# Kernel optimization log

Measured on AMD Instinct MI355X. Metric: run time of the kernel, lower is better.

## Reference

```python
import jax, jax.numpy as jnp
import numpy as np

IN_DIM, OUT_DIM = 256, 64
N_WNODES, N_PNODES, N_EDGES = 100000, 50000, 1600000


def setup_inputs() -> dict:
    key = jax.random.key(0)
    k_h, k_src, k_dst, k_fc, k_attn = jax.random.split(key, 5)
    h = jax.random.normal(k_h, (N_WNODES, IN_DIM), dtype=jnp.float32)
    edge_src = jax.random.randint(k_src, (N_EDGES,), 0, N_WNODES)
    edge_dst = jax.random.randint(k_dst, (N_EDGES,), 0, N_PNODES)
    W_fc = jax.random.normal(k_fc, (IN_DIM, OUT_DIM), dtype=jnp.float32) / np.sqrt(IN_DIM)
    # attn_fc: Linear(2*out_dim, 1, bias=False) -> weight vector of length 2*OUT_DIM
    W_attn = jax.random.normal(k_attn, (2 * OUT_DIM,), dtype=jnp.float32) / np.sqrt(2 * OUT_DIM)
    return {"h": h, "edge_src": edge_src, "edge_dst": edge_dst,
            "n_pnodes": N_PNODES, "W_fc": W_fc, "W_attn": W_attn}


def reference(h, edge_src, edge_dst, n_pnodes, W_fc, W_attn):
    D = W_fc.shape[1]
    z = h @ W_fc                                  # [Nw, D]
    z_src = z[edge_src]                           # [E, D] gather (memory-bound)
    # In the original, only word nodes get 'z'; DGL zero-fills dst 'z', so the
    # dst half of attn_fc contributes nothing: e = leaky_relu(z_src @ a_src + 0 @ a_dst)
    a_src = W_attn[:D]
    e = jax.nn.leaky_relu(z_src @ a_src)          # [E], slope 0.01 matches torch default
    # reduce_func masks zero-valued scores (DGL mailbox padding) with -1000
    e = jnp.where(e == 0.0, -1000.0, e)
    # segment softmax over incoming edges of each destination node
    e_max = jax.ops.segment_max(e, edge_dst, num_segments=n_pnodes)
    e_max = jnp.where(jnp.isfinite(e_max), e_max, 0.0)  # guard empty segments
    w = jnp.exp(e - e_max[edge_dst])              # [E]
    denom = jax.ops.segment_sum(w, edge_dst, num_segments=n_pnodes)
    alpha = w / jnp.maximum(denom[edge_dst], 1e-20)
    # weighted gather-scatter aggregation: sh[dst] = sum alpha * z_src
    h_out = jax.ops.segment_sum(alpha[:, None] * z_src, edge_dst, num_segments=n_pnodes)
    return h_out                                  # [n_pnodes, D] == h[pnode_id]
```

## Files before the change

kernel.cpp:

```cpp
#include <hip/hip_runtime.h>
#include <hip/hip_bf16.h>
#include <math.h>

#define IN_DIM 256
#define OUT_DIM 64
#define CHUNK_LOG2 12
#define BK_LOG2 7
#define MAXNB 512
#define BCAP 6144

typedef __attribute__((ext_vector_type(8))) short short8v;
typedef __attribute__((ext_vector_type(4))) float f32x4;

__device__ __forceinline__ unsigned short f2bf(float f) {
    unsigned u = __float_as_uint(f);
    unsigned r = (u + 0x7fffu + ((u >> 16) & 1u)) >> 16;
    return (unsigned short)r;
}

__device__ __forceinline__ float bf2f(unsigned short b) {
    return __uint_as_float(((unsigned)b) << 16);
}

__device__ __forceinline__ float edge_score(float x) {
    float e = x > 0.0f ? x : 0.01f * x;
    if (e == 0.0f) e = -1000.0f;
    return e;
}

__global__ __launch_bounds__(256) void prep_kernel(
    const float* __restrict__ Wfc, short8v* __restrict__ wtf)
{
    const int v = blockIdx.x * 256 + threadIdx.x;
    const int ks = v >> 8;
    const int t = (v >> 6) & 3;
    const int lane = v & 63;
    const int lg = lane >> 4, lr = lane & 15;
    short8v b;
    #pragma unroll
    for (int j = 0; j < 8; ++j) {
        const int k = ks * 32 + lg * 8 + j;
        b[j] = (short)f2bf(Wfc[k * OUT_DIM + t * 16 + lr]);
    }
    wtf[v] = b;
}

__global__ __launch_bounds__(256, 3) void gemm_s_kernel(
    const float* __restrict__ h, const short8v* __restrict__ wtf,
    const float* __restrict__ Wattn, const int* __restrict__ esrc,
    const int* __restrict__ edst, unsigned short* __restrict__ z,
    float* __restrict__ s, int* __restrict__ bres, int* __restrict__ brec,
    int n_rows, int n_edges, int nb)
{
    __shared__ short hl2[64 * 256];
    const int tid = threadIdx.x;
    const int lane = tid & 63;
    const int wv = tid >> 6;
    const int lg = lane >> 4;
    const int lr = lane & 15;
    const int row0 = blockIdx.x * 64;

    const int nchunks = (n_edges + (1 << CHUNK_LOG2) - 1) >> CHUNK_LOG2;
    const bool hasChunk = blockIdx.x < nchunks;
    const bool fullChunk = hasChunk &&
        ((blockIdx.x << CHUNK_LOG2) + (1 << CHUNK_LOG2) <= n_edges);
    int4 ed[4], es[4];
    if (fullChunk) {
        const int4* ep = (const int4*)edst + (blockIdx.x << (CHUNK_LOG2 - 2));
        const int4* sp = (const int4*)esrc + (blockIdx.x << (CHUNK_LOG2 - 2));
        #pragma unroll
        for (int j = 0; j < 4; ++j) { ed[j] = ep[j * 256 + tid]; es[j] = sp[j * 256 + tid]; }
    }

    float a_attn[4];
    #pragma unroll
    for (int t = 0; t < 4; ++t) a_attn[t] = Wattn[t * 16 + lr];

    #pragma unroll
    for (int i = 0; i < 8; ++i) {
        const int q = i * 256 + tid;
        const int r = q >> 5;
        const int sl = q & 31;
        const int grow = min(row0 + r, n_rows - 1);
        const float4* hp = (const float4*)(h + (size_t)grow * IN_DIM + sl * 8);
        const float4 xa = hp[0];
        const float4 xb = hp[1];
        union { short8v v; __hip_bfloat162 h2[4]; } u;
        u.h2[0] = __float22bfloat162_rn(float2{xa.x, xa.y});
        u.h2[1] = __float22bfloat162_rn(float2{xa.z, xa.w});
        u.h2[2] = __float22bfloat162_rn(float2{xb.x, xb.y});
        u.h2[3] = __float22bfloat162_rn(float2{xb.z, xb.w});
        *(short8v*)((char*)hl2 + r * 512 + ((sl ^ (r & 31)) << 4)) = u.v;
    }
    __syncthreads();

    const int rA = wv * 16 + lr;
    const char* rbase = (const char*)hl2 + rA * 512;
    const int rsw = rA & 31;

    float svj[4] = {0.f, 0.f, 0.f, 0.f};

    #pragma unroll
    for (int hf = 0; hf < 2; ++hf) {
        short8v Bf[8][2];
        #pragma unroll
        for (int ks = 0; ks < 8; ++ks)
            #pragma unroll
            for (int tt = 0; tt < 2; ++tt)
                Bf[ks][tt] = wtf[(ks * 4 + hf * 2 + tt) * 64 + lane];

        f32x4 acc[2];
        acc[0] = (f32x4){0.f, 0.f, 0.f, 0.f};
        acc[1] = (f32x4){0.f, 0.f, 0.f, 0.f};

        #pragma unroll
        for (int ks = 0; ks < 8; ++ks) {
            const short8v av =
                *(const short8v*)(rbase + (((ks * 4 + lg) ^ rsw) << 4));
            acc[0] = __builtin_amdgcn_mfma_f32_16x16x32_bf16(av, Bf[ks][0], acc[0], 0, 0, 0);
            acc[1] = __builtin_amdgcn_mfma_f32_16x16x32_bf16(av, Bf[ks][1], acc[1], 0, 0, 0);
        }

        #pragma unroll
        for (int j = 0; j < 4; ++j) {
            const int row = row0 + wv * 16 + lg * 4 + j;
            const bool ok = row < n_rows;
            #pragma unroll
            for (int tt = 0; tt < 2; ++tt) {
                const int t = hf * 2 + tt;
                const float v = acc[tt][j];
                if (ok) z[(size_t)row * OUT_DIM + t * 16 + lr] =
                    __bfloat16_as_ushort(__float2bfloat16(v));
                svj[j] = fmaf(v, a_attn[t], svj[j]);
            }
        }
    }

    #pragma unroll
    for (int j = 0; j < 4; ++j) {
        const int row = row0 + wv * 16 + lg * 4 + j;
        float p = svj[j];
        #pragma unroll
        for (int o = 1; o < 16; o <<= 1) p += __shfl_xor(p, o);
        if (row < n_rows && lr == 0) s[row] = p;
    }

    __syncthreads();
    int* lcnt = (int*)hl2;
    int* lwoff = lcnt + MAXNB;
    if (hasChunk) {
        for (int j2 = tid; j2 < nb; j2 += 256) lcnt[j2] = 0;
        __syncthreads();
        if (fullChunk) {
            #pragma unroll
            for (int j2 = 0; j2 < 4; ++j2) {
                atomicAdd(&lcnt[ed[j2].x >> BK_LOG2], 1);
                atomicAdd(&lcnt[ed[j2].y >> BK_LOG2], 1);
                atomicAdd(&lcnt[ed[j2].z >> BK_LOG2], 1);
                atomicAdd(&lcnt[ed[j2].w >> BK_LOG2], 1);
            }
        } else {
            const int i0 = blockIdx.x << CHUNK_LOG2;
            const int i1 = min(i0 + (1 << CHUNK_LOG2), n_edges);
            for (int i = i0 + tid; i < i1; i += 256)
                atomicAdd(&lcnt[edst[i] >> BK_LOG2], 1);
        }
        __syncthreads();
        for (int j2 = tid; j2 < nb; j2 += 256) {
            const int cv = lcnt[j2];
            lwoff[j2] = cv ? (j2 * BCAP + atomicAdd(bres + j2, cv)) : 0;
        }
        __syncthreads();
        if (fullChunk) {
            #pragma unroll
            for (int j2 = 0; j2 < 4; ++j2) {
                #define EMIT(dd, ss) { \
                    const int pos = atomicAdd(&lwoff[(dd) >> BK_LOG2], 1); \
                    brec[pos] = (ss) | (((dd) & ((1 << BK_LOG2) - 1)) << 17); }
                EMIT(ed[j2].x, es[j2].x)
                EMIT(ed[j2].y, es[j2].y)
                EMIT(ed[j2].z, es[j2].z)
                EMIT(ed[j2].w, es[j2].w)
                #undef EMIT
            }
        } else {
            const int i0 = blockIdx.x << CHUNK_LOG2;
            const int i1 = min(i0 + (1 << CHUNK_LOG2), n_edges);
            for (int i = i0 + tid; i < i1; i += 256) {
                const int d = edst[i];
                const int pos = atomicAdd(&lwoff[d >> BK_LOG2], 1);
                brec[pos] = esrc[i] | ((d & ((1 << BK_LOG2) - 1)) << 17);
            }
        }
    }
}

__global__ __launch_bounds__(256) void p2_kernel(
    const int* __restrict__ bres, int* __restrict__ brec,
    int2* __restrict__ oln, int n_pnodes)
{
    __shared__ int srec[BCAP];
    __shared__ int lh[128], lsc[128], lwf[128];
    const int b = blockIdx.x;
    const int tid = threadIdx.x;
    const int base = b * BCAP;
    const int len = min(bres[b], BCAP);

    if (tid < 128) lh[tid] = 0;
    __syncthreads();
    for (int i = tid; i < len; i += 256) {
        const int r = brec[base + i];
        srec[i] = r;
        atomicAdd(&lh[r >> 17], 1);
    }
    __syncthreads();
    if (tid < 128) lsc[tid] = lh[tid];
    __syncthreads();
    for (int d = 1; d < 128; d <<= 1) {
        int v = 0;
        if (tid < 128 && tid >= d) v = lsc[tid - d];
        __syncthreads();
        if (tid < 128) lsc[tid] += v;
        __syncthreads();
    }
    const int d0 = b << BK_LOG2;
    if (tid < 128) {
        const int st = lsc[tid] - lh[tid];
        lwf[tid] = st;
        if (d0 + tid < n_pnodes)
            oln[d0 + tid] = make_int2(base + st, lh[tid]);
    }
    __syncthreads();
    for (int i = tid; i < len; i += 256) {
        const int r = srec[i];
        const int pos = atomicAdd(&lwf[r >> 17], 1);
        brec[base + pos] = r & 0x1FFFF;
    }
}

__global__ __launch_bounds__(256) void segment_kernel(
    const int2* __restrict__ oln, const int* __restrict__ ssrc,
    const float* __restrict__ s, const unsigned short* __restrict__ z,
    float* __restrict__ out, int n_pnodes)
{
    const int p = blockIdx.x * 4 + (threadIdx.x >> 6);
    if (p >= n_pnodes) return;
    const int lane = threadIdx.x & 63;
    const int2 ol = oln[p];
    const int beg = ol.x;
    const int len = ol.y;
    const int end = beg + len;

    if (len == 0) {
        out[(size_t)p * OUT_DIM + lane] = 0.0f;
        return;
    }

    float acc = 0.0f, dsum = 0.0f;

    #define GATH1(tt, wsrc, ssrcv) { \
        float wt = __shfl(wsrc, tt); \
        int st = __shfl(ssrcv, tt); \
        acc = fmaf(wt, bf2f(z[(size_t)st * OUT_DIM + lane]), acc); }
    #define GATH8(tt, wsrc, ssrcv) { \
        float w0 = __shfl(wsrc, tt),     w1 = __shfl(wsrc, tt + 1); \
        float w2 = __shfl(wsrc, tt + 2), w3 = __shfl(wsrc, tt + 3); \
        float w4 = __shfl(wsrc, tt + 4), w5 = __shfl(wsrc, tt + 5); \
        float w6 = __shfl(wsrc, tt + 6), w7 = __shfl(wsrc, tt + 7); \
        int a0 = __shfl(ssrcv, tt),     a1 = __shfl(ssrcv, tt + 1); \
        int a2 = __shfl(ssrcv, tt + 2), a3 = __shfl(ssrcv, tt + 3); \
        int a4 = __shfl(ssrcv, tt + 4), a5 = __shfl(ssrcv, tt + 5); \
        int a6 = __shfl(ssrcv, tt + 6), a7 = __shfl(ssrcv, tt + 7); \
        float z0 = bf2f(z[(size_t)a0 * OUT_DIM + lane]); \
        float z1 = bf2f(z[(size_t)a1 * OUT_DIM + lane]); \
        float z2 = bf2f(z[(size_t)a2 * OUT_DIM + lane]); \
        float z3 = bf2f(z[(size_t)a3 * OUT_DIM + lane]); \
        float z4 = bf2f(z[(size_t)a4 * OUT_DIM + lane]); \
        float z5 = bf2f(z[(size_t)a5 * OUT_DIM + lane]); \
        float z6 = bf2f(z[(size_t)a6 * OUT_DIM + lane]); \
        float z7 = bf2f(z[(size_t)a7 * OUT_DIM + lane]); \
        acc = fmaf(w0, z0, acc); acc = fmaf(w1, z1, acc); \
        acc = fmaf(w2, z2, acc); acc = fmaf(w3, z3, acc); \
        acc = fmaf(w4, z4, acc); acc = fmaf(w5, z5, acc); \
        acc = fmaf(w6, z6, acc); acc = fmaf(w7, z7, acc); }

    if (len <= 64) {
        const bool v = lane < len;
        const int j = beg + (v ? lane : 0);
        const int sr = ssrc[j];
        const float e = v ? edge_score(s[sr]) : -INFINITY;
        float m = e;
        #pragma unroll
        for (int o = 32; o > 0; o >>= 1) m = fmaxf(m, __shfl_xor(m, o));
        float w = v ? __expf(e - m) : 0.0f;
        dsum = w;
        #pragma unroll
        for (int o = 32; o > 0; o >>= 1) dsum += __shfl_xor(dsum, o);

        int t = 0;
        for (; t + 8 <= len; t += 8) GATH8(t, w, sr)
        for (; t < len; ++t) GATH1(t, w, sr)
    } else {
        float m = -INFINITY;
        for (int j = beg + lane; j < end; j += 64)
            m = fmaxf(m, edge_score(s[ssrc[j]]));
        #pragma unroll
        for (int o = 32; o > 0; o >>= 1) m = fmaxf(m, __shfl_xor(m, o));

        for (int c = beg; c < end; c += 64) {
            const int j = c + lane;
            float w = 0.0f;
            int sr = 0;
            if (j < end) {
                sr = ssrc[j];
                w = __expf(edge_score(s[sr]) - m);
            }
            dsum += w;
            const int cn = min(64, end - c);
            int t = 0;
            for (; t + 8 <= cn; t += 8) GATH8(t, w, sr)
            for (; t < cn; ++t) GATH1(t, w, sr)
        }
        #pragma unroll
        for (int o = 32; o > 0; o >>= 1) dsum += __shfl_xor(dsum, o);
    }
    #undef GATH8
    #undef GATH1

    out[(size_t)p * OUT_DIM + lane] = acc / fmaxf(dsum, 1e-20f);
}

extern "C" void kernel_launch(void* const* d_in, const int* in_sizes, int n_in,
                              void* d_out, int out_size, void* d_ws, size_t ws_size,
                              hipStream_t stream)
{
    const float* h     = (const float*)d_in[0];
    const int*   esrc  = (const int*)d_in[1];
    const int*   edst  = (const int*)d_in[2];
    const float* Wfc   = (const float*)d_in[4];
    const float* Wattn = (const float*)d_in[5];
    float* out = (float*)d_out;

    const int n_w = in_sizes[0] / IN_DIM;
    const int n_e = in_sizes[1];
    const int n_p = out_size / OUT_DIM;
    const int nb  = (n_p + (1 << BK_LOG2) - 1) >> BK_LOG2;

    short8v* wtf            = (short8v*)d_ws;
    unsigned short* z       = (unsigned short*)(wtf + 2048);
    float* s                = (float*)(z + (size_t)n_w * OUT_DIM);
    int* brec               = (int*)(s + n_w);
    int2* oln               = (int2*)(brec + (size_t)nb * BCAP);
    int* bres               = (int*)(oln + n_p);

    hipMemsetAsync(bres, 0, (size_t)nb * sizeof(int), stream);

    prep_kernel<<<8, 256, 0, stream>>>(Wfc, wtf);
    const int gemm_blocks = (n_w + 63) / 64;
    gemm_s_kernel<<<gemm_blocks, 256, 0, stream>>>(h, wtf, Wattn, esrc, edst,
                                                   z, s, bres, brec, n_w, n_e, nb);
    p2_kernel<<<nb, 256, 0, stream>>>(bres, brec, oln, n_p);
    segment_kernel<<<(n_p + 3) / 4, 256, 0, stream>>>(oln, brec, s, z, out, n_p);
}
```

Before: 111.0 us.

## Process four row tiles per GEMM block with double-buffered LDS pipelining

Result: no change. 111.1 us (+0.1%).

```diff
diff --git a/kernel.cpp b/kernel.cpp
--- a/kernel.cpp
+++ b/kernel.cpp
@@ -45,109 +45,129 @@
     wtf[v] = b;
 }
 
-__global__ __launch_bounds__(256, 3) void gemm_s_kernel(
+__global__ __launch_bounds__(256, 2) void gemm_s_kernel(
     const float* __restrict__ h, const short8v* __restrict__ wtf,
     const float* __restrict__ Wattn, const int* __restrict__ esrc,
     const int* __restrict__ edst, unsigned short* __restrict__ z,
     float* __restrict__ s, int* __restrict__ bres, int* __restrict__ brec,
     int n_rows, int n_edges, int nb)
 {
-    __shared__ short hl2[64 * 256];
+    __shared__ short hlA[64 * 256];
+    __shared__ short hlB[64 * 256];
+    __shared__ int ltab[2 * MAXNB];
     const int tid = threadIdx.x;
     const int lane = tid & 63;
     const int wv = tid >> 6;
     const int lg = lane >> 4;
     const int lr = lane & 15;
-    const int row0 = blockIdx.x * 64;
-
-    const int nchunks = (n_edges + (1 << CHUNK_LOG2) - 1) >> CHUNK_LOG2;
-    const bool hasChunk = blockIdx.x < nchunks;
-    const bool fullChunk = hasChunk &&
-        ((blockIdx.x << CHUNK_LOG2) + (1 << CHUNK_LOG2) <= n_edges);
-    int4 ed[4], es[4];
-    if (fullChunk) {
-        const int4* ep = (const int4*)edst + (blockIdx.x << (CHUNK_LOG2 - 2));
-        const int4* sp = (const int4*)esrc + (blockIdx.x << (CHUNK_LOG2 - 2));
-        #pragma unroll
-        for (int j = 0; j < 4; ++j) { ed[j] = ep[j * 256 + tid]; es[j] = sp[j * 256 + tid]; }
-    }
+    const int brow0 = blockIdx.x * 256;
+
+    short8v Bf[8][4];
+    #pragma unroll
+    for (int ks = 0; ks < 8; ++ks)
+        #pragma unroll
+        for (int t = 0; t < 4; ++t)
+            Bf[ks][t] = wtf[(ks * 4 + t) * 64 + lane];
 
     float a_attn[4];
     #pragma unroll
     for (int t = 0; t < 4; ++t) a_attn[t] = Wattn[t * 16 + lr];
 
-    #pragma unroll
-    for (int i = 0; i < 8; ++i) {
-        const int q = i * 256 + tid;
-        const int r = q >> 5;
-        const int sl = q & 31;
-        const int grow = min(row0 + r, n_rows - 1);
-        const float4* hp = (const float4*)(h + (size_t)grow * IN_DIM + sl * 8);
-        const float4 xa = hp[0];
-        const float4 xb = hp[1];
-        union { short8v v; __hip_bfloat162 h2[4]; } u;
-        u.h2[0] = __float22bfloat162_rn(float2{xa.x, xa.y});
-        u.h2[1] = __float22bfloat162_rn(float2{xa.z, xa.w});
-        u.h2[2] = __float22bfloat162_rn(float2{xb.x, xb.y});
-        u.h2[3] = __float22bfloat162_rn(float2{xb.z, xb.w});
-        *(short8v*)((char*)hl2 + r * 512 + ((sl ^ (r & 31)) << 4)) = u.v;
-    }
-    __syncthreads();
-
-    const int rA = wv * 16 + lr;
-    const char* rbase = (const char*)hl2 + rA * 512;
-    const int rsw = rA & 31;
-
-    float svj[4] = {0.f, 0.f, 0.f, 0.f};
-
-    #pragma unroll
-    for (int hf = 0; hf < 2; ++hf) {
-        short8v Bf[8][2];
-        #pragma unroll
-        for (int ks = 0; ks < 8; ++ks)
-            #pragma unroll
-            for (int tt = 0; tt < 2; ++tt)
-                Bf[ks][tt] = wtf[(ks * 4 + hf * 2 + tt) * 64 + lane];
-
-        f32x4 acc[2];
-        acc[0] = (f32x4){0.f, 0.f, 0.f, 0.f};
-        acc[1] = (f32x4){0.f, 0.f, 0.f, 0.f};
-
+    short8v sreg[8];
+
+    auto LOADT = [&](int t) {
+        #pragma unroll
+        for (int i = 0; i < 8; ++i) {
+            const int q = i * 256 + tid;
+            const int r = q >> 5;
+            const int sl = q & 31;
+            const int grow = min(brow0 + t * 64 + r, n_rows - 1);
+            const float4* hp = (const float4*)(h + (size_t)grow * IN_DIM + sl * 8);
+            const float4 xa = hp[0];
+            const float4 xb = hp[1];
+            union { short8v v; __hip_bfloat162 h2[4]; } u;
+            u.h2[0] = __float22bfloat162_rn(float2{xa.x, xa.y});
+            u.h2[1] = __float22bfloat162_rn(float2{xa.z, xa.w});
+            u.h2[2] = __float22bfloat162_rn(float2{xb.x, xb.y});
+            u.h2[3] = __float22bfloat162_rn(float2{xb.z, xb.w});
+            sreg[i] = u.v;
+        }
+    };
+
+    auto WRITET = [&](short* buf) {
+        #pragma unroll
+        for (int i = 0; i < 8; ++i) {
+            const int q = i * 256 + tid;
+            const int r = q >> 5;
+            const int sl = q & 31;
+            *(short8v*)((char*)buf + r * 512 + ((sl ^ (r & 31)) << 4)) = sreg[i];
+        }
+    };
+
+    auto COMPUTE = [&](const short* buf, int t) {
+        f32x4 acc[4];
+        #pragma unroll
+        for (int tt = 0; tt < 4; ++tt) acc[tt] = (f32x4){0.f, 0.f, 0.f, 0.f};
+        const int rA = wv * 16 + lr;
+        const char* rbase = (const char*)buf + rA * 512;
+        const int rsw = rA & 31;
         #pragma unroll
         for (int ks = 0; ks < 8; ++ks) {
-            const short8v av =
-                *(const short8v*)(rbase + (((ks * 4 + lg) ^ rsw) << 4));
-            acc[0] = __builtin_amdgcn_mfma_f32_16x16x32_bf16(av, Bf[ks][0], acc[0], 0, 0, 0);
-            acc[1] = __builtin_amdgcn_mfma_f32_16x16x32_bf16(av, Bf[ks][1], acc[1], 0, 0, 0);
-        }
-
+            const short8v av = *(const short8v*)(rbase + (((ks * 4 + lg) ^ rsw) << 4));
+            #pragma unroll
+            for (int tt = 0; tt < 4; ++tt)
+                acc[tt] = __builtin_amdgcn_mfma_f32_16x16x32_bf16(av, Bf[ks][tt], acc[tt], 0, 0, 0);
+        }
         #pragma unroll
         for (int j = 0; j < 4; ++j) {
-            const int row = row0 + wv * 16 + lg * 4 + j;
+            const int row = brow0 + t * 64 + wv * 16 + lg * 4 + j;
             const bool ok = row < n_rows;
-            #pragma unroll
-            for (int tt = 0; tt < 2; ++tt) {
-                const int t = hf * 2 + tt;
+            float sv = 0.0f;
+            #pragma unroll
+            for (int tt = 0; tt < 4; ++tt) {
                 const float v = acc[tt][j];
-                if (ok) z[(size_t)row * OUT_DIM + t * 16 + lr] =
+                if (ok) z[(size_t)row * OUT_DIM + tt * 16 + lr] =
                     __bfloat16_as_ushort(__float2bfloat16(v));
-                svj[j] = fmaf(v, a_attn[t], svj[j]);
-            }
-        }
-    }
-
-    #pragma unroll
-    for (int j = 0; j < 4; ++j) {
-        const int row = row0 + wv * 16 + lg * 4 + j;
-        float p = svj[j];
-        #pragma unroll
-        for (int o = 1; o < 16; o <<= 1) p += __shfl_xor(p, o);
-        if (row < n_rows && lr == 0) s[row] = p;
-    }
-
-    __syncthreads();
-    int* lcnt = (int*)hl2;
-    int* lwoff = lcnt + MAXNB;
+                sv = fmaf(v, a_attn[tt], sv);
+            }
+            #pragma unroll
+            for (int o = 1; o < 16; o <<= 1) sv += __shfl_xor(sv, o);
+            if (ok && lr == 0) s[row] = sv;
+        }
+    };
+
+    LOADT(0);
+    WRITET(hlA);
+    __syncthreads();
+    LOADT(1);
+    COMPUTE(hlA, 0);
+    WRITET(hlB);
+    __syncthreads();
+    LOADT(2);
+    COMPUTE(hlB, 1);
+    WRITET(hlA);
+    __syncthreads();
+    LOADT(3);
+    COMPUTE(hlA, 2);
+    WRITET(hlB);
+    __syncthreads();
+
+    const int i0 = blockIdx.x << CHUNK_LOG2;
+    const int i1 = min(i0 + (1 << CHUNK_LOG2), n_edges);
+    const bool hasChunk = i0 < n_edges;
+    const bool fullChunk = hasChunk && (i0 + (1 << CHUNK_LOG2) <= n_edges);
+    int4 ed[4], es[4];
+    if (fullChunk) {
+        const int4* ep = (const int4*)edst + (i0 >> 2);
+        const int4* sp = (const int4*)esrc + (i0 >> 2);
+        #pragma unroll
+        for (int j = 0; j < 4; ++j) { ed[j] = ep[j * 256 + tid]; es[j] = sp[j * 256 + tid]; }
+    }
+
+    COMPUTE(hlB, 3);
+
+    int* lcnt = ltab;
+    int* lwoff = ltab + MAXNB;
     if (hasChunk) {
         for (int j2 = tid; j2 < nb; j2 += 256) lcnt[j2] = 0;
         __syncthreads();
@@ -160,8 +180,6 @@
                 atomicAdd(&lcnt[ed[j2].w >> BK_LOG2], 1);
             }
         } else {
-            const int i0 = blockIdx.x << CHUNK_LOG2;
-            const int i1 = min(i0 + (1 << CHUNK_LOG2), n_edges);
             for (int i = i0 + tid; i < i1; i += 256)
                 atomicAdd(&lcnt[edst[i] >> BK_LOG2], 1);
         }
@@ -184,8 +202,6 @@
                 #undef EMIT
             }
         } else {
-            const int i0 = blockIdx.x << CHUNK_LOG2;
-            const int i1 = min(i0 + (1 << CHUNK_LOG2), n_edges);
             for (int i = i0 + tid; i < i1; i += 256) {
                 const int d = edst[i];
                 const int pos = atomicAdd(&lwoff[d >> BK_LOG2], 1);
@@ -356,7 +372,8 @@
     hipMemsetAsync(bres, 0, (size_t)nb * sizeof(int), stream);
 
     prep_kernel<<<8, 256, 0, stream>>>(Wfc, wtf);
-    const int gemm_blocks = (n_w + 63) / 64;
+    const int nchunks = (n_e + (1 << CHUNK_LOG2) - 1) >> CHUNK_LOG2;
+    const int gemm_blocks = max((n_w + 255) / 256, nchunks);
     gemm_s_kernel<<<gemm_blocks, 256, 0, stream>>>(h, wtf, Wattn, esrc, edst,
                                                    z, s, bres, brec, n_w, n_e, nb);
     p2_kernel<<<nb, 256, 0, stream>>>(bres, brec, oln, n_p);
```
